# Optimization experiments

Measured on AMD Instinct MI355X. Metric: run time of the kernel, lower is better.

## Reference

```python
import jax, jax.numpy as jnp
import numpy as np
from jax import lax

DIM = 256; HEADS = 16; DHEAD = 16; H = 12; W = 26
DS = 4; KOFF = 6; OSCALE = 4.0
SCALE = DHEAD ** -0.5
EPS = 1e-5


def _create_grid(hh, ww, dtype):
    # channel0 = x (width index), channel1 = y (height index); matches torch meshgrid(arange(w), arange(h), indexing='xy')
    gy, gx = jnp.meshgrid(jnp.arange(hh, dtype=dtype), jnp.arange(ww, dtype=dtype), indexing='ij')
    return jnp.stack([gx, gy], axis=0)  # (2, hh, ww)


def _grid_sample_bilinear(img, grid):
    # F.grid_sample, mode='bilinear', padding_mode='zeros', align_corners=False
    # img (B,C,Hi,Wi); grid (B,Ho,Wo,2), grid[...,0]=x-norm, grid[...,1]=y-norm in [-1,1]
    B, C, Hi, Wi = img.shape
    x = ((grid[..., 0] + 1.0) * Wi - 1.0) / 2.0
    y = ((grid[..., 1] + 1.0) * Hi - 1.0) / 2.0
    x0 = jnp.floor(x); y0 = jnp.floor(y)

    def gather(xi, yi):
        valid = ((xi >= 0) & (xi < Wi) & (yi >= 0) & (yi < Hi)).astype(img.dtype)
        xc = jnp.clip(xi, 0, Wi - 1).astype(jnp.int32)
        yc = jnp.clip(yi, 0, Hi - 1).astype(jnp.int32)
        v = jax.vmap(lambda im, yy, xx: im[:, yy, xx])(img, yc, xc)  # (B,C,Ho,Wo)
        return v * valid[:, None]

    wx1 = (x - x0)[:, None]; wx0 = 1.0 - wx1
    wy1 = (y - y0)[:, None]; wy0 = 1.0 - wy1
    return (gather(x0, y0) * wy0 * wx0 + gather(x0 + 1.0, y0) * wy0 * wx1
            + gather(x0, y0 + 1.0) * wy1 * wx0 + gather(x0 + 1.0, y0 + 1.0) * wy1 * wx1)


def _forward(x, q, w_off_dw, b_off_dw, w_off_pw, wk, wv, w_out, b_out,
             cpb_w1, cpb_b1, cpb_w2, cpb_b2, cpb_w3, cpb_b3,
             conv1d_w, conv1d_b, ln_g, ln_b):
    b = x.shape[0]
    # faithful to torch: q.repeat(1,1,h*w).view(bs,1,dim,h,w).squeeze(1) == tile then reshape
    q_map = jnp.tile(q[:, 0, :], (1, H * W)).reshape(b, DIM, H, W)

    # to_offsets: depthwise Conv2d(k=6,s=4,p=1) -> GELU -> 1x1 conv (no bias) -> tanh -> *offset_scale
    t = lax.conv_general_dilated(q_map, w_off_dw, window_strides=(DS, DS),
                                 padding=[(1, 1), (1, 1)], feature_group_count=DIM,
                                 dimension_numbers=('NCHW', 'OIHW', 'NCHW'))
    t = jax.nn.gelu(t + b_off_dw[None, :, None, None], approximate=False)
    off = jnp.tanh(jnp.einsum('oc,bchw->bohw', w_off_pw, t)) * OSCALE  # (b,2,Hk,Wk)
    Hk, Wk = off.shape[-2], off.shape[-1]  # 3, 6

    gkv = _create_grid(Hk, Wk, x.dtype)
    vg0 = gkv[0] + off[:, 0]
    vg1 = gkv[1] + off[:, 1]
    # faithful repo normalize_grid: channel0 / (h-1), channel1 / (w-1)
    n0 = 2.0 * vg0 / max(Hk - 1, 1) - 1.0
    n1 = 2.0 * vg1 / max(Wk - 1, 1) - 1.0
    vgrid_scaled = jnp.stack([n0, n1], axis=-1)  # (b, Hk, Wk, 2)

    kv = _grid_sample_bilinear(x, vgrid_scaled)  # (b, DIM, Hk, Wk)
    k = jnp.einsum('oc,bchw->bohw', wk, kv)
    v = jnp.einsum('oc,bchw->bohw', wv, kv)

    qh = (q_map * SCALE).reshape(b, HEADS, DHEAD, H * W).transpose(0, 1, 3, 2)  # (b,h,i,d)
    kh = k.reshape(b, HEADS, DHEAD, Hk * Wk).transpose(0, 1, 3, 2)              # (b,h,j,d)
    vh = v.reshape(b, HEADS, DHEAD, Hk * Wk).transpose(0, 1, 3, 2)
    sim = jnp.einsum('bhid,bhjd->bhij', qh, kh)  # (b,16,312,18)

    # CPB relative position bias
    gq = _create_grid(H, W, x.dtype)
    gq0 = 2.0 * gq[0] / max(H - 1, 1) - 1.0
    gq1 = 2.0 * gq[1] / max(W - 1, 1) - 1.0
    grid_q = jnp.stack([gq0, gq1], axis=-1).reshape(1, H * W, 2)
    grid_kv = vgrid_scaled.reshape(b, Hk * Wk, 2)
    pos = grid_q[:, :, None, :] - grid_kv[:, None, :, :]       # (b,i,j,2)
    bias = jnp.sign(pos) * jnp.log(jnp.abs(pos) + 1.0)
    bias = jax.nn.relu(bias @ cpb_w1.T + cpb_b1)
    bias = jax.nn.relu(bias @ cpb_w2.T + cpb_b2)
    bias = bias @ cpb_w3.T + cpb_b3                             # (b,i,j,heads)
    sim = sim + bias.transpose(0, 3, 1, 2)

    attn = jax.nn.softmax(sim, axis=-1)  # dropout(0.1) identity in eval
    out = jnp.einsum('bhij,bhjd->bhid', attn, vh)               # (b,h,i,d)
    out = out.transpose(0, 1, 3, 2).reshape(b, DIM, H, W)        # 'b h (x y) d -> b (h d) x y'
    out = jnp.einsum('oc,bchw->bohw', w_out, out) + b_out[None, :, None, None]

    # SpatialCrossAttention tail: view -> permute -> Conv1d(312,1,1) -> residual -> LayerNorm
    tokens = out.reshape(b, DIM, H * W).transpose(0, 2, 1)       # (b,312,256)
    pooled = jnp.einsum('t,btc->bc', conv1d_w, tokens)[:, None, :] + conv1d_b[None, :, None]
    y = pooled + q
    mu = y.mean(-1, keepdims=True)
    var = y.var(-1, keepdims=True)
    return (y - mu) / jnp.sqrt(var + EPS) * ln_g + ln_b          # (b,1,256)


def setup_inputs() -> dict:
    key = jax.random.key(0)
    ks = jax.random.split(key, 16)
    rn = lambda i, shape, s=0.02: jax.random.normal(ks[i], shape, dtype=jnp.float32) * s
    B = 256
    return {
        'x': jax.random.normal(ks[0], (B, DIM, H, W), dtype=jnp.float32),
        'q': jax.random.normal(ks[1], (B, 1, DIM), dtype=jnp.float32),
        'w_off_dw': rn(2, (DIM, 1, KOFF, KOFF), 0.05),
        'b_off_dw': jnp.zeros((DIM,), jnp.float32),
        'w_off_pw': rn(3, (2, DIM), 0.05),
        'wk': rn(4, (DIM, DIM)),
        'wv': rn(5, (DIM, DIM)),
        'w_out': rn(6, (DIM, DIM)),
        'b_out': jnp.zeros((DIM,), jnp.float32),
        'cpb_w1': rn(7, (64, 2), 0.1),
        'cpb_b1': jnp.zeros((64,), jnp.float32),
        'cpb_w2': rn(8, (64, 64), 0.1),
        'cpb_b2': jnp.zeros((64,), jnp.float32),
        'cpb_w3': rn(9, (HEADS, 64), 0.1),
        'cpb_b3': jnp.zeros((HEADS,), jnp.float32),
        'conv1d_w': rn(10, (H * W,), 0.05),
        'conv1d_b': jnp.zeros((1,), jnp.float32),
        'ln_g': jnp.ones((DIM,), jnp.float32),
        'ln_b': jnp.zeros((DIM,), jnp.float32),
    }


def reference(x, q, w_off_dw, b_off_dw, w_off_pw, wk, wv, w_out, b_out,
              cpb_w1, cpb_b1, cpb_w2, cpb_b2, cpb_w3, cpb_b3,
              conv1d_w, conv1d_b, ln_g, ln_b):
    return _forward(x, q, w_off_dw, b_off_dw, w_off_pw, wk, wv, w_out, b_out,
                    cpb_w1, cpb_b1, cpb_w2, cpb_b2, cpb_w3, cpb_b3,
                    conv1d_w, conv1d_b, ln_g, ln_b)
```

## Files before the change

### kernel.cpp

```cpp
#include <hip/hip_runtime.h>
#include <math.h>


typedef __attribute__((ext_vector_type(8))) short short8;
typedef __attribute__((ext_vector_type(4))) float floatx4;

union U16 { uint4 u; short8 s; };

__device__ __forceinline__ unsigned int f2bf(float f) {
    unsigned int u = __float_as_uint(f);
    u += 0x7fffu + ((u >> 16) & 1u);
    return u >> 16;
}
__device__ __forceinline__ unsigned int pk2(float a, float b) {
    return f2bf(a) | (f2bf(b) << 16);
}
__device__ __forceinline__ float bf2f(unsigned short v) {
    return __uint_as_float((unsigned int)v << 16);
}

#define WSF_W2 16384
#define WSF_W3 16896
#define WSF_DW 68096

__global__ __launch_bounds__(256) void k0_setup(
    const float* __restrict__ wk, const float* __restrict__ wv,
    const float* __restrict__ cw2, const float* __restrict__ cw3,
    const float* __restrict__ w_dw, unsigned int* __restrict__ ws)
{
    const int t = blockIdx.x * 256 + threadIdx.x;
    uint4* ws4 = (uint4*)ws;
    {
        const int m2 = t >> 13;
        const int r = t & 8191;
        const int mt = r >> 9, ks = (r >> 6) & 7, lane = r & 63;
        const int nn = lane & 15, qd = lane >> 4;
        const float* src = (m2 ? wv : wk) + (mt * 16 + nn) * 256 + ks * 32 + qd * 8;
        uint4 o;
        o.x = pk2(src[0], src[1]); o.y = pk2(src[2], src[3]);
        o.z = pk2(src[4], src[5]); o.w = pk2(src[6], src[7]);
        ws4[t] = o;
    }
    if (t < 512) {
        const int mt = t >> 7, ks = (t >> 6) & 1, lane = t & 63;
        const int nn = lane & 15, qd = lane >> 4;
        const float* src = cw2 + (mt * 16 + nn) * 64 + ks * 32 + qd * 8;
        uint4 o;
        o.x = pk2(src[0], src[1]); o.y = pk2(src[2], src[3]);
        o.z = pk2(src[4], src[5]); o.w = pk2(src[6], src[7]);
        ws4[WSF_W2 + t] = o;
    }
    if (t < 128) {
        const int ks = t >> 6, lane = t & 63;
        const int nn = lane & 15, qd = lane >> 4;
        const float* src = cw3 + nn * 64 + ks * 32 + qd * 8;
        uint4 o;
        o.x = pk2(src[0], src[1]); o.y = pk2(src[2], src[3]);
        o.z = pk2(src[4], src[5]); o.w = pk2(src[6], src[7]);
        ws4[WSF_W3 + t] = o;
    }
    float* wsf = (float*)ws;
    for (int k = t; k < 9216; k += 16384) {
        const int c = k / 36, i = k - c * 36;
        wsf[WSF_DW + i * 256 + c] = w_dw[k];
    }
}

__global__ __launch_bounds__(512, 2) void k_fused(
    const float* __restrict__ x, const float* __restrict__ q,
    const float* __restrict__ b_dw, const float* __restrict__ w_pw,
    const float* __restrict__ cw1, const float* __restrict__ cb1,
    const float* __restrict__ cb2, const float* __restrict__ cb3,
    const float* __restrict__ conv_w, const float* __restrict__ conv_b,
    const float* __restrict__ w_out, const float* __restrict__ b_out,
    const float* __restrict__ ln_g, const float* __restrict__ ln_b,
    const unsigned int* __restrict__ ws, float* __restrict__ out)
{
    const int b = blockIdx.x, tid = threadIdx.x;
    const int w = tid >> 6, lane = tid & 63;
    const int n = lane & 15, qd = lane >> 4;

    __shared__ float qf_s[256];
    __shared__ unsigned short q_sb[256];
    __shared__ unsigned short v_sb[5120];
    __shared__ float F0[468], F1[216];
    __shared__ unsigned int lutxy[312];
    __shared__ float off_s[36], n0_s[18], n1_s[18];
    __shared__ float sx0[18], sy0[18], swx[18], swy[18];
    __shared__ float wA_s[288];
    __shared__ __align__(16) float m_s[256];
    __shared__ float pooled_s[256], redb[16];
    __shared__ __align__(16) unsigned char UB[38464];
    float* S_ = (float*)UB;
    unsigned short* kvT = (unsigned short*)UB;
    float* qsw = (float*)UB;
    float* t_s = (float*)(UB + 16512);
    unsigned short* k_sb = (unsigned short*)(UB + 20000);
    unsigned int* h2w = (unsigned int*)(UB + 20000);

    const uint4* ws4 = (const uint4*)ws;
    const float* wsf = (const float*)ws;

    uint4 W2f[4][2], W3f[2];
    #pragma unroll
    for (int mtl = 0; mtl < 4; ++mtl)
        #pragma unroll
        for (int ks = 0; ks < 2; ++ks)
            W2f[mtl][ks] = ws4[WSF_W2 + mtl * 128 + ks * 64 + lane];
    W3f[0] = ws4[WSF_W3 + lane];
    W3f[1] = ws4[WSF_W3 + 64 + lane];

    float W1a[16], W1b[16], B1r[16];
    #pragma unroll
    for (int kk = 0; kk < 16; ++kk) {
        const int kid = (kk < 8) ? (qd * 8 + kk) : (32 + qd * 8 + kk - 8);
        W1a[kk] = cw1[kid * 2]; W1b[kk] = cw1[kid * 2 + 1]; B1r[kk] = cb1[kid];
    }
    float bb2[16];
    #pragma unroll
    for (int mtl = 0; mtl < 4; ++mtl)
        #pragma unroll
        for (int r = 0; r < 4; ++r) bb2[mtl * 4 + r] = cb2[mtl * 16 + qd * 4 + r];
    float bb3[4];
    #pragma unroll
    for (int r = 0; r < 4; ++r) bb3[r] = cb3[qd * 4 + r];

    if (tid < 256) {
        const float qv = q[b * 256 + tid];
        qf_s[tid] = qv;
        q_sb[tid] = (unsigned short)f2bf(qv * 0.25f);
    }
    for (int u = tid; u < 4128; u += 512) {
        const int r = u / 258, i = u - r * 258;
        qsw[u] = (i < 256) ? q[b * 256 + i] : 0.f;
    }
    for (int u = tid; u < 312; u += 512) {
        const int iy = u / 26;
        lutxy[u] = (unsigned int)(u - iy * 26) | ((unsigned int)iy << 16);
    }
    __syncthreads();

    {
        const int c = tid & 255, g = tid >> 8;
        float wreg[36];
        #pragma unroll
        for (int i = 0; i < 36; ++i) wreg[i] = wsf[WSF_DW + i * 256 + c];
        float acc[9];
        const float bv = b_dw[c];
        #pragma unroll
        for (int a = 0; a < 9; ++a) acc[a] = bv;
        const int cb = (c * 56) & 255;
        const int cp = (c & 15) * 258;
        for (int jh = 0; jh < 3; ++jh) {
            for (int kh = 0; kh < 6; ++kh) {
                const int ih = jh * 4 - 1 + kh;
                if (ih < 0 || ih >= 12) continue;
                const int rb = ih * 26;
                #pragma unroll
                for (int jwl = 0; jwl < 3; ++jwl) {
                    const int jw = g * 3 + jwl;
                    #pragma unroll
                    for (int kw = 0; kw < 6; ++kw) {
                        const int iw = jw * 4 - 1 + kw;
                        if (iw < 0 || iw >= 26) continue;
                        acc[jh * 3 + jwl] += wreg[kh * 6 + kw] * qsw[cp + ((cb + rb + iw) & 255)];
                    }
                }
            }
        }
        #pragma unroll
        for (int a = 0; a < 9; ++a) {
            const int jh = a / 3, jwl = a - jh * 3;
            const int p = jh * 6 + g * 3 + jwl;
            const float v = acc[a];
            t_s[p * 256 + c] = 0.5f * v * (1.0f + erff(v * 0.70710678118654752f));
        }
    }
    __syncthreads();

    for (int oi = w; oi < 36; oi += 8) {
        const int o = oi / 18, p = oi - o * 18;
        float s = 0.f;
        for (int c = lane; c < 256; c += 64) s += w_pw[o * 256 + c] * t_s[p * 256 + c];
        for (int d = 32; d > 0; d >>= 1) s += __shfl_down(s, d, 64);
        if (lane == 0) off_s[oi] = 4.0f * tanhf(s);
    }
    __syncthreads();

    if (tid < 18) {
        const int j = tid, jh = j / 6, jw = j - jh * 6;
        const float vg0 = (float)jw + off_s[j];
        const float vg1 = (float)jh + off_s[18 + j];
        const float n0 = 2.0f * vg0 / 2.0f - 1.0f;
        const float n1 = 2.0f * vg1 / 5.0f - 1.0f;
        n0_s[j] = n0; n1_s[j] = n1;
        const float xp = ((n0 + 1.0f) * 26.0f - 1.0f) * 0.5f;
        const float yp = ((n1 + 1.0f) * 12.0f - 1.0f) * 0.5f;
        const float x0 = floorf(xp), y0 = floorf(yp);
        sx0[j] = x0; sy0[j] = y0; swx[j] = xp - x0; swy[j] = yp - y0;
    }
    __syncthreads();

    {
        const int c = tid & 255, g = tid >> 8;
        const float* xb = x + ((size_t)b * 256 + c) * 312;
        for (int jj = 0; jj < 9; ++jj) {
            const int j = g * 9 + jj;
            const int x0 = (int)sx0[j], y0 = (int)sy0[j];
            const int x1 = x0 + 1, y1 = y0 + 1;
            const float wx1 = swx[j], wy1 = swy[j];
            const float wx0 = 1.f - wx1, wy0 = 1.f - wy1;
            const bool xv0 = (x0 >= 0) & (x0 < 26), xv1 = (x1 >= 0) & (x1 < 26);
            const bool yv0 = (y0 >= 0) & (y0 < 12), yv1 = (y1 >= 0) & (y1 < 12);
            const float v00 = (xv0 & yv0) ? xb[y0 * 26 + x0] : 0.f;
            const float v01 = (xv1 & yv0) ? xb[y0 * 26 + x1] : 0.f;
            const float v10 = (xv0 & yv1) ? xb[y1 * 26 + x0] : 0.f;
            const float v11 = (xv1 & yv1) ? xb[y1 * 26 + x1] : 0.f;
            const float val = wy0 * (wx0 * v00 + wx1 * v01) + wy1 * (wx0 * v10 + wx1 * v11);
            kvT[j * 264 + c] = (unsigned short)f2bf(val);
        }
    }
    for (int u = tid; u < 684; u += 512) {
        if (u < 468) {
            const int ixv = u / 18, j = u - ixv * 18;
            const float p0 = (float)ixv * (2.0f / 11.0f) - 1.0f - n0_s[j];
            F0[u] = copysignf(__logf(1.0f + fabsf(p0)), p0);
        } else {
            const int u2 = u - 468;
            const int iyv = u2 / 18, j = u2 - iyv * 18;
            const float p1 = (float)iyv * (2.0f / 25.0f) - 1.0f - n1_s[j];
            F1[u2] = copysignf(__logf(1.0f + fabsf(p1)), p1);
        }
    }
    __syncthreads();

    {
        const int m2 = w & 1, mtb = w >> 1;
        floatx4 pa[4][2];
        #pragma unroll
        for (int a = 0; a < 4; ++a) {
            pa[a][0] = (floatx4){0.f, 0.f, 0.f, 0.f};
            pa[a][1] = (floatx4){0.f, 0.f, 0.f, 0.f};
        }
        for (int ks = 0; ks < 8; ++ks) {
            U16 b0, b1;
            b0.u = *(const uint4*)(kvT + n * 264 + ks * 32 + qd * 8);
            b1.u = make_uint4(0u, 0u, 0u, 0u);
            if (n < 2) b1.u = *(const uint4*)(kvT + (16 + n) * 264 + ks * 32 + qd * 8);
            #pragma unroll
            for (int mtl = 0; mtl < 4; ++mtl) {
                const int mt = mtb + mtl * 4;
                U16 A; A.u = ws4[m2 * 8192 + mt * 512 + ks * 64 + lane];
                pa[mtl][0] = __builtin_amdgcn_mfma_f32_16x16x32_bf16(A.s, b0.s, pa[mtl][0], 0, 0, 0);
                pa[mtl][1] = __builtin_amdgcn_mfma_f32_16x16x32_bf16(A.s, b1.s, pa[mtl][1], 0, 0, 0);
            }
        }
        unsigned short* dst = m2 ? v_sb : k_sb;
        #pragma unroll
        for (int mtl = 0; mtl < 4; ++mtl) {
            const int mt = mtb + mtl * 4;
            #pragma unroll
            for (int r = 0; r < 4; ++r) {
                const int o = mt * 16 + qd * 4 + r;
                dst[o * 20 + n] = (unsigned short)f2bf(pa[mtl][0][r]);
                if (n < 2) dst[o * 20 + 16 + n] = (unsigned short)f2bf(pa[mtl][1][r]);
            }
        }
    }
    __syncthreads();

    uint4 BkU[2][2];
    #pragma unroll
    for (int hh = 0; hh < 2; ++hh)
        #pragma unroll
        for (int jt = 0; jt < 2; ++jt) {
            unsigned int u0 = 0, u1 = 0, u2 = 0, u3 = 0;
            if (qd < 2 && (jt == 0 || n < 2)) {
                const int h = w * 2 + hh;
                const int j = jt * 16 + n;
                const int cb0 = (h * 16 + qd * 8) * 20 + j;
                u0 = (unsigned)k_sb[cb0] | ((unsigned)k_sb[cb0 + 20] << 16);
                u1 = (unsigned)k_sb[cb0 + 40] | ((unsigned)k_sb[cb0 + 60] << 16);
                u2 = (unsigned)k_sb[cb0 + 80] | ((unsigned)k_sb[cb0 + 100] << 16);
                u3 = (unsigned)k_sb[cb0 + 120] | ((unsigned)k_sb[cb0 + 140] << 16);
            }
            BkU[hh][jt] = make_uint4(u0, u1, u2, u3);
        }
    __syncthreads();

    float wAcc[18];
    #pragma unroll
    for (int j = 0; j < 18; ++j) wAcc[j] = 0.f;

    for (int ch = 0; ch < 20; ++ch) {
        const int ibase = ch * 16;
        const int CI = (ch == 19) ? 8 : 16;

        #pragma unroll
        for (int hh = 0; hh < 2; ++hh) {
            const int h = w * 2 + hh;
            unsigned int a0 = 0, a1 = 0, a2 = 0, a3u = 0;
            if (qd < 2) {
                const int base = h * 16 + qd * 8;
                a0 = (unsigned)q_sb[((base + 0) * 56 + ibase + n) & 255] |
                     ((unsigned)q_sb[((base + 1) * 56 + ibase + n) & 255] << 16);
                a1 = (unsigned)q_sb[((base + 2) * 56 + ibase + n) & 255] |
                     ((unsigned)q_sb[((base + 3) * 56 + ibase + n) & 255] << 16);
                a2 = (unsigned)q_sb[((base + 4) * 56 + ibase + n) & 255] |
                     ((unsigned)q_sb[((base + 5) * 56 + ibase + n) & 255] << 16);
                a3u = (unsigned)q_sb[((base + 6) * 56 + ibase + n) & 255] |
                      ((unsigned)q_sb[((base + 7) * 56 + ibase + n) & 255] << 16);
            }
            U16 Af; Af.u = make_uint4(a0, a1, a2, a3u);
            #pragma unroll
            for (int jt = 0; jt < 2; ++jt) {
                U16 Bf; Bf.u = BkU[hh][jt];
                floatx4 D = {0.f, 0.f, 0.f, 0.f};
                D = __builtin_amdgcn_mfma_f32_16x16x32_bf16(Af.s, Bf.s, D, 0, 0, 0);
                const int j = jt * 16 + n;
                if (j < 18) {
                    #pragma unroll
                    for (int r = 0; r < 4; ++r)
                        S_[((qd * 4 + r) * 18 + j) * 17 + h] = D[r];
                }
            }
        }
        __syncthreads();

        {
            const int i0 = ibase + n;
            const unsigned int lv = lutxy[i0 < 312 ? i0 : 311];
            const int ix = (int)(lv & 0xffffu), iy = (int)(lv >> 16);
            for (int nt = w; nt < 18; nt += 8) {
                const float f0 = F0[ix * 18 + nt];
                const float f1 = F1[iy * 18 + nt];
                float h1v[16];
                #pragma unroll
                for (int kk = 0; kk < 16; ++kk)
                    h1v[kk] = fmaxf(fmaf(W1a[kk], f0, fmaf(W1b[kk], f1, B1r[kk])), 0.f);
                U16 ub0, ub1;
                ub0.u = make_uint4(pk2(h1v[0], h1v[1]), pk2(h1v[2], h1v[3]),
                                   pk2(h1v[4], h1v[5]), pk2(h1v[6], h1v[7]));
                ub1.u = make_uint4(pk2(h1v[8], h1v[9]), pk2(h1v[10], h1v[11]),
                                   pk2(h1v[12], h1v[13]), pk2(h1v[14], h1v[15]));
                floatx4 g2[4];
                #pragma unroll
                for (int mtl = 0; mtl < 4; ++mtl) {
                    U16 A0; A0.u = W2f[mtl][0];
                    U16 A1; A1.u = W2f[mtl][1];
                    floatx4 acc = {0.f, 0.f, 0.f, 0.f};
                    acc = __builtin_amdgcn_mfma_f32_16x16x32_bf16(A0.s, ub0.s, acc, 0, 0, 0);
                    acc = __builtin_amdgcn_mfma_f32_16x16x32_bf16(A1.s, ub1.s, acc, 0, 0, 0);
                    g2[mtl] = acc;
                }
                unsigned int* hw = h2w + w * 576 + n * 36;
                #pragma unroll
                for (int mtl = 0; mtl < 4; ++mtl) {
                    const float e0 = fmaxf(g2[mtl][0] + bb2[mtl * 4 + 0], 0.f);
                    const float e1 = fmaxf(g2[mtl][1] + bb2[mtl * 4 + 1], 0.f);
                    const float e2 = fmaxf(g2[mtl][2] + bb2[mtl * 4 + 2], 0.f);
                    const float e3 = fmaxf(g2[mtl][3] + bb2[mtl * 4 + 3], 0.f);
                    hw[mtl * 8 + qd * 2]     = pk2(e0, e1);
                    hw[mtl * 8 + qd * 2 + 1] = pk2(e2, e3);
                }
                U16 uc0, uc1;
                uc0.u = *(const uint4*)(hw + qd * 4);
                uc1.u = *(const uint4*)(hw + 16 + qd * 4);
                floatx4 a3 = {0.f, 0.f, 0.f, 0.f};
                {
                    U16 A0; A0.u = W3f[0]; U16 A1; A1.u = W3f[1];
                    a3 = __builtin_amdgcn_mfma_f32_16x16x32_bf16(A0.s, uc0.s, a3, 0, 0, 0);
                    a3 = __builtin_amdgcn_mfma_f32_16x16x32_bf16(A1.s, uc1.s, a3, 0, 0, 0);
                }
                float* sp = S_ + (n * 18 + nt) * 17 + qd * 4;
                #pragma unroll
                for (int r = 0; r < 4; ++r) sp[r] = a3[r] + bb3[r] + sp[r];
            }
        }
        __syncthreads();

        if (tid < 256) {
            const int il = tid >> 4, h = tid & 15;
            if (il < CI) {
                float lv[18];
                #pragma unroll
                for (int j = 0; j < 18; ++j) lv[j] = S_[(il * 18 + j) * 17 + h];
                float m = lv[0];
                #pragma unroll
                for (int j = 1; j < 18; ++j) m = fmaxf(m, lv[j]);
                float s = 0.f;
                #pragma unroll
                for (int j = 0; j < 18; ++j) { lv[j] = __expf(lv[j] - m); s += lv[j]; }
                const float wgt = conv_w[ibase + il] / s;
                #pragma unroll
                for (int j = 0; j < 18; ++j) wAcc[j] = fmaf(wgt, lv[j], wAcc[j]);
            }
        }
        __syncthreads();
    }

    if (tid < 256) {
        const int il = tid >> 4, h = tid & 15;
        float* wred = (float*)UB;
        #pragma unroll
        for (int j = 0; j < 18; ++j) wred[(il * 16 + h) * 18 + j] = wAcc[j];
    }
    __syncthreads();
    {
        const float* wred = (const float*)UB;
        for (int u = tid; u < 288; u += 512) {
            const int h = u / 18, j = u - h * 18;
            float s = 0.f;
            #pragma unroll
            for (int il = 0; il < 16; ++il) s += wred[(il * 16 + h) * 18 + j];
            wA_s[u] = s;
        }
    }
    {
        float v = 0.f;
        for (int u = tid; u < 312; u += 512) v += conv_w[u];
        for (int d = 32; d > 0; d >>= 1) v += __shfl_down(v, d, 64);
        if (lane == 0) redb[w] = v;
    }
    __syncthreads();

    if (tid < 256) {
        const int c = tid;
        const int hb = (c >> 4) * 18;
        float acc = 0.f;
        #pragma unroll
        for (int j = 0; j < 18; ++j) acc += wA_s[hb + j] * bf2f(v_sb[c * 20 + j]);
        m_s[c] = acc;
    }
    __syncthreads();

    const float Ssum = redb[0] + redb[1] + redb[2] + redb[3] +
                       redb[4] + redb[5] + redb[6] + redb[7];

    {
        const float4 mm = *(const float4*)(m_s + lane * 4);
        for (int ol = 0; ol < 32; ++ol) {
            const int o = w * 32 + ol;
            const float4 wq = *(const float4*)(w_out + o * 256 + lane * 4);
            float d = wq.x * mm.x + wq.y * mm.y + wq.z * mm.z + wq.w * mm.w;
            for (int dd = 32; dd > 0; dd >>= 1) d += __shfl_down(d, dd, 64);
            if (lane == 0) pooled_s[o] = d;
        }
    }
    __syncthreads();

    if (tid < 256) {
        const int o = tid;
        const float y = pooled_s[o] + b_out[o] * Ssum + conv_b[0] + qf_s[o];
        float s1 = y, s2 = y * y;
        for (int d = 32; d > 0; d >>= 1) { s1 += __shfl_down(s1, d, 64); s2 += __shfl_down(s2, d, 64); }
        if (lane == 0) { redb[8 + w] = s1; redb[12 + w] = s2; }
    }
    __syncthreads();
    if (tid < 256) {
        const int o = tid;
        const float y = pooled_s[o] + b_out[o] * Ssum + conv_b[0] + qf_s[o];
        const float S1 = redb[8] + redb[9] + redb[10] + redb[11];
        const float S2 = redb[12] + redb[13] + redb[14] + redb[15];
        const float mu = S1 * (1.0f / 256.0f);
        const float var = S2 * (1.0f / 256.0f) - mu * mu;
        out[b * 256 + o] = (y - mu) * rsqrtf(var + 1e-5f) * ln_g[o] + ln_b[o];
    }
}

extern "C" void kernel_launch(void* const* d_in, const int* in_sizes, int n_in,
                              void* d_out, int out_size, void* d_ws, size_t ws_size,
                              hipStream_t stream) {
    const float* x       = (const float*)d_in[0];
    const float* q       = (const float*)d_in[1];
    const float* w_dw    = (const float*)d_in[2];
    const float* b_dwp   = (const float*)d_in[3];
    const float* w_pw    = (const float*)d_in[4];
    const float* wk      = (const float*)d_in[5];
    const float* wv      = (const float*)d_in[6];
    const float* w_out   = (const float*)d_in[7];
    const float* b_out   = (const float*)d_in[8];
    const float* cw1     = (const float*)d_in[9];
    const float* cb1     = (const float*)d_in[10];
    const float* cw2     = (const float*)d_in[11];
    const float* cb2     = (const float*)d_in[12];
    const float* cw3     = (const float*)d_in[13];
    const float* cb3     = (const float*)d_in[14];
    const float* conv_w  = (const float*)d_in[15];
    const float* conv_b  = (const float*)d_in[16];
    const float* ln_g    = (const float*)d_in[17];
    const float* ln_b    = (const float*)d_in[18];
    float* out = (float*)d_out;
    unsigned int* ws = (unsigned int*)d_ws;

    k0_setup<<<64, 256, 0, stream>>>(wk, wv, cw2, cw3, w_dw, ws);
    k_fused<<<256, 512, 0, stream>>>(x, q, b_dwp, w_pw, cw1, cb1, cb2, cb3,
                                     conv_w, conv_b, w_out, b_out, ln_g, ln_b,
                                     (const unsigned int*)ws, out);
}
```

Baseline: 268.1 us.

## Split per-batch attention over two blocks with atomic reduction and separate final kernel

The fused per-batch kernel now launches two blocks per batch element, each covering half of the 312 spatial positions, and reduces their per-head weight sums into workspace with atomicAdd. The output projection, conv bias and LayerNorm move into a new k3_final kernel that reads V (stored in fp32 to workspace) and the reduced weights. Bias registers are replaced by shared-memory loads to lower register pressure. This doubles the grid to fill more CUs, at the cost of recomputing the offsets/K/V stages in both blocks, an extra launch, and global atomics.

```diff
diff --git a/kernel.cpp b/kernel.cpp
--- a/kernel.cpp
+++ b/kernel.cpp
@@ -15,13 +15,12 @@
 __device__ __forceinline__ unsigned int pk2(float a, float b) {
     return f2bf(a) | (f2bf(b) << 16);
 }
-__device__ __forceinline__ float bf2f(unsigned short v) {
-    return __uint_as_float((unsigned int)v << 16);
-}
 
 #define WSF_W2 16384
 #define WSF_W3 16896
 #define WSF_DW 68096
+#define WSF_V  80000
+#define WSF_WA 1260000
 
 __global__ __launch_bounds__(256) void k0_setup(
     const float* __restrict__ wk, const float* __restrict__ wv,
@@ -64,6 +63,7 @@
         const int c = k / 36, i = k - c * 36;
         wsf[WSF_DW + i * 256 + c] = w_dw[k];
     }
+    for (int u = t; u < 73728; u += 16384) wsf[WSF_WA + u] = 0.f;
 }
 
 __global__ __launch_bounds__(512, 2) void k_fused(
@@ -71,35 +71,32 @@
     const float* __restrict__ b_dw, const float* __restrict__ w_pw,
     const float* __restrict__ cw1, const float* __restrict__ cb1,
     const float* __restrict__ cb2, const float* __restrict__ cb3,
-    const float* __restrict__ conv_w, const float* __restrict__ conv_b,
-    const float* __restrict__ w_out, const float* __restrict__ b_out,
-    const float* __restrict__ ln_g, const float* __restrict__ ln_b,
-    const unsigned int* __restrict__ ws, float* __restrict__ out)
+    const float* __restrict__ conv_w,
+    unsigned int* __restrict__ ws)
 {
-    const int b = blockIdx.x, tid = threadIdx.x;
+    const int ib = blockIdx.x;
+    const int b = blockIdx.y, tid = threadIdx.x;
     const int w = tid >> 6, lane = tid & 63;
     const int n = lane & 15, qd = lane >> 4;
 
-    __shared__ float qf_s[256];
     __shared__ unsigned short q_sb[256];
-    __shared__ unsigned short v_sb[5120];
     __shared__ float F0[468], F1[216];
     __shared__ unsigned int lutxy[312];
     __shared__ float off_s[36], n0_s[18], n1_s[18];
     __shared__ float sx0[18], sy0[18], swx[18], swy[18];
-    __shared__ float wA_s[288];
-    __shared__ __align__(16) float m_s[256];
-    __shared__ float pooled_s[256], redb[16];
+    __shared__ float b2_s[64], b3_s[16];
     __shared__ __align__(16) unsigned char UB[38464];
     float* S_ = (float*)UB;
     unsigned short* kvT = (unsigned short*)UB;
     float* qsw = (float*)UB;
     float* t_s = (float*)(UB + 16512);
-    unsigned short* k_sb = (unsigned short*)(UB + 20000);
+    unsigned short* k_sb = (unsigned short*)(UB + 16512);
     unsigned int* h2w = (unsigned int*)(UB + 20000);
+    float* wred = (float*)UB;
 
     const uint4* ws4 = (const uint4*)ws;
     const float* wsf = (const float*)ws;
+    float* wsw = (float*)ws;
 
     uint4 W2f[4][2], W3f[2];
     #pragma unroll
@@ -116,28 +113,18 @@
         const int kid = (kk < 8) ? (qd * 8 + kk) : (32 + qd * 8 + kk - 8);
         W1a[kk] = cw1[kid * 2]; W1b[kk] = cw1[kid * 2 + 1]; B1r[kk] = cb1[kid];
     }
-    float bb2[16];
-    #pragma unroll
-    for (int mtl = 0; mtl < 4; ++mtl)
-        #pragma unroll
-        for (int r = 0; r < 4; ++r) bb2[mtl * 4 + r] = cb2[mtl * 16 + qd * 4 + r];
-    float bb3[4];
-    #pragma unroll
-    for (int r = 0; r < 4; ++r) bb3[r] = cb3[qd * 4 + r];
-
-    if (tid < 256) {
-        const float qv = q[b * 256 + tid];
-        qf_s[tid] = qv;
-        q_sb[tid] = (unsigned short)f2bf(qv * 0.25f);
-    }
+
+    if (tid < 256) q_sb[tid] = (unsigned short)f2bf(q[b * 256 + tid] * 0.25f);
     for (int u = tid; u < 4128; u += 512) {
         const int r = u / 258, i = u - r * 258;
         qsw[u] = (i < 256) ? q[b * 256 + i] : 0.f;
     }
-    for (int u = tid; u < 312; u += 512) {
-        const int iy = u / 26;
-        lutxy[u] = (unsigned int)(u - iy * 26) | ((unsigned int)iy << 16);
-    }
+    if (tid < 312) {
+        const int iy = tid / 26;
+        lutxy[tid] = (unsigned int)(tid - iy * 26) | ((unsigned int)iy << 16);
+    }
+    if (tid < 64) b2_s[tid] = cb2[tid];
+    if (tid < 16) b3_s[tid] = cb3[tid];
     __syncthreads();
 
     {
@@ -255,15 +242,28 @@
                 pa[mtl][1] = __builtin_amdgcn_mfma_f32_16x16x32_bf16(A.s, b1.s, pa[mtl][1], 0, 0, 0);
             }
         }
-        unsigned short* dst = m2 ? v_sb : k_sb;
-        #pragma unroll
-        for (int mtl = 0; mtl < 4; ++mtl) {
-            const int mt = mtb + mtl * 4;
+        if (m2 == 0) {
             #pragma unroll
-            for (int r = 0; r < 4; ++r) {
-                const int o = mt * 16 + qd * 4 + r;
-                dst[o * 20 + n] = (unsigned short)f2bf(pa[mtl][0][r]);
-                if (n < 2) dst[o * 20 + 16 + n] = (unsigned short)f2bf(pa[mtl][1][r]);
+            for (int mtl = 0; mtl < 4; ++mtl) {
+                const int mt = mtb + mtl * 4;
+                #pragma unroll
+                for (int r = 0; r < 4; ++r) {
+                    const int o = mt * 16 + qd * 4 + r;
+                    k_sb[o * 20 + n] = (unsigned short)f2bf(pa[mtl][0][r]);
+                    if (n < 2) k_sb[o * 20 + 16 + n] = (unsigned short)f2bf(pa[mtl][1][r]);
+                }
+            }
+        } else if (ib == 0) {
+            float* vdst = wsw + WSF_V + (size_t)b * 4608;
+            #pragma unroll
+            for (int mtl = 0; mtl < 4; ++mtl) {
+                const int mt = mtb + mtl * 4;
+                #pragma unroll
+                for (int r = 0; r < 4; ++r) {
+                    const int o = mt * 16 + qd * 4 + r;
+                    vdst[o * 18 + n] = pa[mtl][0][r];
+                    if (n < 2) vdst[o * 18 + 16 + n] = pa[mtl][1][r];
+                }
             }
         }
     }
@@ -292,9 +292,10 @@
     #pragma unroll
     for (int j = 0; j < 18; ++j) wAcc[j] = 0.f;
 
-    for (int ch = 0; ch < 20; ++ch) {
-        const int ibase = ch * 16;
-        const int CI = (ch == 19) ? 8 : 16;
+    for (int ch = 0; ch < 10; ++ch) {
+        const int ibase = ib * 160 + ch * 16;
+        const int CI = (312 - ibase < 16) ? (312 - ibase) : 16;
+        if (CI <= 0) break;
 
         #pragma unroll
         for (int hh = 0; hh < 2; ++hh) {
@@ -334,32 +335,27 @@
             for (int nt = w; nt < 18; nt += 8) {
                 const float f0 = F0[ix * 18 + nt];
                 const float f1 = F1[iy * 18 + nt];
-                float h1v[16];
-                #pragma unroll
-                for (int kk = 0; kk < 16; ++kk)
-                    h1v[kk] = fmaxf(fmaf(W1a[kk], f0, fmaf(W1b[kk], f1, B1r[kk])), 0.f);
+                unsigned int uu[8];
+                #pragma unroll
+                for (int kp = 0; kp < 8; ++kp) {
+                    const float ha = fmaxf(fmaf(W1a[2 * kp], f0, fmaf(W1b[2 * kp], f1, B1r[2 * kp])), 0.f);
+                    const float hb = fmaxf(fmaf(W1a[2 * kp + 1], f0, fmaf(W1b[2 * kp + 1], f1, B1r[2 * kp + 1])), 0.f);
+                    uu[kp] = pk2(ha, hb);
+                }
                 U16 ub0, ub1;
-                ub0.u = make_uint4(pk2(h1v[0], h1v[1]), pk2(h1v[2], h1v[3]),
-                                   pk2(h1v[4], h1v[5]), pk2(h1v[6], h1v[7]));
-                ub1.u = make_uint4(pk2(h1v[8], h1v[9]), pk2(h1v[10], h1v[11]),
-                                   pk2(h1v[12], h1v[13]), pk2(h1v[14], h1v[15]));
-                floatx4 g2[4];
+                ub0.u = make_uint4(uu[0], uu[1], uu[2], uu[3]);
+                ub1.u = make_uint4(uu[4], uu[5], uu[6], uu[7]);
+                unsigned int* hw = h2w + w * 576 + n * 36;
                 #pragma unroll
                 for (int mtl = 0; mtl < 4; ++mtl) {
-                    U16 A0; A0.u = W2f[mtl][0];
-                    U16 A1; A1.u = W2f[mtl][1];
+                    U16 A0, A1; A0.u = W2f[mtl][0]; A1.u = W2f[mtl][1];
                     floatx4 acc = {0.f, 0.f, 0.f, 0.f};
                     acc = __builtin_amdgcn_mfma_f32_16x16x32_bf16(A0.s, ub0.s, acc, 0, 0, 0);
                     acc = __builtin_amdgcn_mfma_f32_16x16x32_bf16(A1.s, ub1.s, acc, 0, 0, 0);
-                    g2[mtl] = acc;
-                }
-                unsigned int* hw = h2w + w * 576 + n * 36;
-                #pragma unroll
-                for (int mtl = 0; mtl < 4; ++mtl) {
-                    const float e0 = fmaxf(g2[mtl][0] + bb2[mtl * 4 + 0], 0.f);
-                    const float e1 = fmaxf(g2[mtl][1] + bb2[mtl * 4 + 1], 0.f);
-                    const float e2 = fmaxf(g2[mtl][2] + bb2[mtl * 4 + 2], 0.f);
-                    const float e3 = fmaxf(g2[mtl][3] + bb2[mtl * 4 + 3], 0.f);
+                    const float e0 = fmaxf(acc[0] + b2_s[mtl * 16 + qd * 4 + 0], 0.f);
+                    const float e1 = fmaxf(acc[1] + b2_s[mtl * 16 + qd * 4 + 1], 0.f);
+                    const float e2 = fmaxf(acc[2] + b2_s[mtl * 16 + qd * 4 + 2], 0.f);
+                    const float e3 = fmaxf(acc[3] + b2_s[mtl * 16 + qd * 4 + 3], 0.f);
                     hw[mtl * 8 + qd * 2]     = pk2(e0, e1);
                     hw[mtl * 8 + qd * 2 + 1] = pk2(e2, e3);
                 }
@@ -368,13 +364,13 @@
                 uc1.u = *(const uint4*)(hw + 16 + qd * 4);
                 floatx4 a3 = {0.f, 0.f, 0.f, 0.f};
                 {
-                    U16 A0; A0.u = W3f[0]; U16 A1; A1.u = W3f[1];
+                    U16 A0, A1; A0.u = W3f[0]; A1.u = W3f[1];
                     a3 = __builtin_amdgcn_mfma_f32_16x16x32_bf16(A0.s, uc0.s, a3, 0, 0, 0);
                     a3 = __builtin_amdgcn_mfma_f32_16x16x32_bf16(A1.s, uc1.s, a3, 0, 0, 0);
                 }
                 float* sp = S_ + (n * 18 + nt) * 17 + qd * 4;
                 #pragma unroll
-                for (int r = 0; r < 4; ++r) sp[r] = a3[r] + bb3[r] + sp[r];
+                for (int r = 0; r < 4; ++r) sp[r] = a3[r] + b3_s[qd * 4 + r] + sp[r];
             }
         }
         __syncthreads();
@@ -400,72 +396,75 @@
     }
 
     if (tid < 256) {
-        const int il = tid >> 4, h = tid & 15;
-        float* wred = (float*)UB;
-        #pragma unroll
-        for (int j = 0; j < 18; ++j) wred[(il * 16 + h) * 18 + j] = wAcc[j];
-    }
-    __syncthreads();
+        const int slot = tid >> 4, h = tid & 15;
+        #pragma unroll
+        for (int j = 0; j < 18; ++j) wred[(slot * 16 + h) * 18 + j] = wAcc[j];
+    }
+    __syncthreads();
+    for (int u = tid; u < 288; u += 512) {
+        const int h = u / 18, j = u - h * 18;
+        float s = 0.f;
+        #pragma unroll
+        for (int sl = 0; sl < 16; ++sl) s += wred[(sl * 16 + h) * 18 + j];
+        atomicAdd(&wsw[WSF_WA + b * 288 + u], s);
+    }
+}
+
+__global__ __launch_bounds__(256) void k3_final(
+    const float* __restrict__ q,
+    const float* __restrict__ w_out, const float* __restrict__ b_out,
+    const float* __restrict__ conv_w, const float* __restrict__ conv_b,
+    const float* __restrict__ ln_g, const float* __restrict__ ln_b,
+    const float* __restrict__ ws, float* __restrict__ out)
+{
+    const int b = blockIdx.x, tid = threadIdx.x;
+    __shared__ float wA_s[288];
+    __shared__ __align__(16) float m_s[256];
+    __shared__ float redS[4], redA[4], redB[4];
+
+    for (int i = tid; i < 288; i += 256) wA_s[i] = ws[WSF_WA + b * 288 + i];
+    __syncthreads();
+
     {
-        const float* wred = (const float*)UB;
-        for (int u = tid; u < 288; u += 512) {
-            const int h = u / 18, j = u - h * 18;
-            float s = 0.f;
-            #pragma unroll
-            for (int il = 0; il < 16; ++il) s += wred[(il * 16 + h) * 18 + j];
-            wA_s[u] = s;
-        }
+        const int c = tid;
+        const float* vr = ws + WSF_V + (size_t)b * 4608 + c * 18;
+        const float* wr = &wA_s[(c >> 4) * 18];
+        float acc = 0.f;
+        #pragma unroll
+        for (int j = 0; j < 18; ++j) acc += wr[j] * vr[j];
+        m_s[c] = acc;
     }
     {
-        float v = 0.f;
-        for (int u = tid; u < 312; u += 512) v += conv_w[u];
-        for (int d = 32; d > 0; d >>= 1) v += __shfl_down(v, d, 64);
-        if (lane == 0) redb[w] = v;
-    }
-    __syncthreads();
-
-    if (tid < 256) {
-        const int c = tid;
-        const int hb = (c >> 4) * 18;
-        float acc = 0.f;
-        #pragma unroll
-        for (int j = 0; j < 18; ++j) acc += wA_s[hb + j] * bf2f(v_sb[c * 20 + j]);
-        m_s[c] = acc;
-    }
-    __syncthreads();
-
-    const float Ssum = redb[0] + redb[1] + redb[2] + redb[3] +
-                       redb[4] + redb[5] + redb[6] + redb[7];
-
-    {
-        const float4 mm = *(const float4*)(m_s + lane * 4);
-        for (int ol = 0; ol < 32; ++ol) {
-            const int o = w * 32 + ol;
-            const float4 wq = *(const float4*)(w_out + o * 256 + lane * 4);
-            float d = wq.x * mm.x + wq.y * mm.y + wq.z * mm.z + wq.w * mm.w;
-            for (int dd = 32; dd > 0; dd >>= 1) d += __shfl_down(d, dd, 64);
-            if (lane == 0) pooled_s[o] = d;
-        }
-    }
-    __syncthreads();
-
-    if (tid < 256) {
-        const int o = tid;
-        const float y = pooled_s[o] + b_out[o] * Ssum + conv_b[0] + qf_s[o];
-        float s1 = y, s2 = y * y;
-        for (int d = 32; d > 0; d >>= 1) { s1 += __shfl_down(s1, d, 64); s2 += __shfl_down(s2, d, 64); }
-        if (lane == 0) { redb[8 + w] = s1; redb[12 + w] = s2; }
-    }
-    __syncthreads();
-    if (tid < 256) {
-        const int o = tid;
-        const float y = pooled_s[o] + b_out[o] * Ssum + conv_b[0] + qf_s[o];
-        const float S1 = redb[8] + redb[9] + redb[10] + redb[11];
-        const float S2 = redb[12] + redb[13] + redb[14] + redb[15];
-        const float mu = S1 * (1.0f / 256.0f);
-        const float var = S2 * (1.0f / 256.0f) - mu * mu;
-        out[b * 256 + o] = (y - mu) * rsqrtf(var + 1e-5f) * ln_g[o] + ln_b[o];
-    }
+        float sp = conv_w[tid] + ((tid + 256) < 312 ? conv_w[tid + 256] : 0.f);
+        for (int d = 32; d > 0; d >>= 1) sp += __shfl_down(sp, d, 64);
+        if ((tid & 63) == 0) redS[tid >> 6] = sp;
+    }
+    __syncthreads();
+    const float S = redS[0] + redS[1] + redS[2] + redS[3];
+
+    const int o = tid;
+    float acc = b_out[o] * S + conv_b[0];
+    const float4* wor = (const float4*)(w_out + o * 256);
+    const float4* m4 = (const float4*)m_s;
+    for (int c4 = 0; c4 < 64; ++c4) {
+        const float4 wq = wor[c4];
+        const float4 mq = m4[c4];
+        acc += wq.x * mq.x + wq.y * mq.y + wq.z * mq.z + wq.w * mq.w;
+    }
+    const float y = acc + q[b * 256 + o];
+
+    float s1 = y, s2 = y * y;
+    for (int d = 32; d > 0; d >>= 1) {
+        s1 += __shfl_down(s1, d, 64);
+        s2 += __shfl_down(s2, d, 64);
+    }
+    if ((tid & 63) == 0) { redA[tid >> 6] = s1; redB[tid >> 6] = s2; }
+    __syncthreads();
+    const float S1 = redA[0] + redA[1] + redA[2] + redA[3];
+    const float S2 = redB[0] + redB[1] + redB[2] + redB[3];
+    const float mu = S1 * (1.0f / 256.0f);
+    const float var = S2 * (1.0f / 256.0f) - mu * mu;
+    out[b * 256 + o] = (y - mu) * rsqrtf(var + 1e-5f) * ln_g[o] + ln_b[o];
 }
 
 extern "C" void kernel_launch(void* const* d_in, const int* in_sizes, int n_in,
@@ -494,7 +493,8 @@
     unsigned int* ws = (unsigned int*)d_ws;
 
     k0_setup<<<64, 256, 0, stream>>>(wk, wv, cw2, cw3, w_dw, ws);
-    k_fused<<<256, 512, 0, stream>>>(x, q, b_dwp, w_pw, cw1, cb1, cb2, cb3,
-                                     conv_w, conv_b, w_out, b_out, ln_g, ln_b,
-                                     (const unsigned int*)ws, out);
+    k_fused<<<dim3(2, 256), 512, 0, stream>>>(x, q, b_dwp, w_pw, cw1, cb1, cb2, cb3,
+                                              conv_w, ws);
+    k3_final<<<256, 256, 0, stream>>>(q, w_out, b_out, conv_w, conv_b, ln_g, ln_b,
+                                      (const float*)ws, out);
 }
```

Result: slower. 340.7 us (+27.1%).
